# Performance work log

Measured on AMD Instinct MI355X. Metric: run time of the kernel, lower is better.

Reference implementation:

```python
import jax, jax.numpy as jnp
import numpy as np

EPS = 1e-5  # torch LayerNorm default

def _ln(x, g, b):
    mu = jnp.mean(x, -1, keepdims=True)
    var = jnp.mean((x - mu) ** 2, -1, keepdims=True)
    return (x - mu) * jax.lax.rsqrt(var + EPS) * g + b

def _xavier(key, shape):
    fan_in, fan_out = shape[-2], shape[-1]
    s = (2.0 / (fan_in + fan_out)) ** 0.5
    return jax.random.normal(key, shape, dtype=jnp.float32) * s

def setup_inputs() -> dict:
    key = jax.random.key(0)
    ks = jax.random.split(key, 24)
    N, E, B = 10000, 160000, 64
    D, M, FF, K = 128, 32, 32, 5
    EIN = 2 * FF + 1 + 2 * D          # 321
    inp = {}
    inp["coords"] = jax.random.normal(ks[0], (N, 3), dtype=jnp.float32)
    inp["atomids"] = jax.random.randint(ks[1], (N,), 0, 11)
    inp["edge_index"] = jax.random.randint(ks[2], (2, E), 0, N)
    inp["batch"] = jnp.sort(jax.random.randint(ks[3], (N,), 0, B))
    inp["num_graphs"] = B
    inp["emb"] = _xavier(ks[4], (11, D))
    # stacked per-kernel EGNN params (leading dim K=5)
    inp["keW1"] = _xavier(ks[5], (K, EIN, 2 * EIN)); inp["keb1"] = jnp.zeros((K, 2 * EIN))
    inp["keW2"] = _xavier(ks[6], (K, 2 * EIN, M));   inp["keb2"] = jnp.zeros((K, M))
    inp["keng"] = jnp.ones((K, M));   inp["kenb"] = jnp.zeros((K, M))
    inp["kn1g"] = jnp.ones((K, D));   inp["kn1b"] = jnp.zeros((K, D))
    inp["knW1"] = _xavier(ks[7], (K, D + M, 2 * D)); inp["knb1"] = jnp.zeros((K, 2 * D))
    inp["knW2"] = _xavier(ks[8], (K, 2 * D, D));     inp["knb2"] = jnp.zeros((K, D))
    inp["kn2g"] = jnp.ones((K, D));   inp["kn2b"] = jnp.zeros((K, D))
    # fnn: (K+1)*D = 768 -> 256 -> 256 -> 256
    inp["fW0"] = _xavier(ks[9], ((K + 1) * D, 256)); inp["fb0"] = jnp.zeros((256,))
    inp["fW1"] = _xavier(ks[10], (256, 256));        inp["fb1"] = jnp.zeros((256,))
    inp["fW2"] = _xavier(ks[11], (256, 256));        inp["fb2"] = jnp.zeros((256,))
    # fnn2: 256 -> 256 -> 256 -> 1
    inp["gW0"] = _xavier(ks[12], (256, 256));        inp["gb0"] = jnp.zeros((256,))
    inp["gW1"] = _xavier(ks[13], (256, 256));        inp["gb1"] = jnp.zeros((256,))
    inp["gW2"] = _xavier(ks[14], (256, 1));          inp["gb2"] = jnp.zeros((1,))
    return inp

def reference(coords, atomids, edge_index, batch, num_graphs, emb,
              keW1, keb1, keW2, keb2, keng, kenb, kn1g, kn1b,
              knW1, knb1, knW2, knb2, kn2g, kn2b,
              fW0, fb0, fW1, fb1, fW2, fb2,
              gW0, gb0, gW1, gb1, gW2, gb2):
    silu = jax.nn.silu
    N = coords.shape[0]
    src, dst = edge_index[0], edge_index[1]  # x_j = x[src], x_i = x[dst]
    feats = emb[atomids]                                  # [N,128]
    # coords are never updated across kernels -> fourier edge attr computed once
    rel = coords[src] - coords[dst]                       # [E,3]
    d = jnp.sum(rel * rel, -1, keepdims=True)             # [E,1] squared distance
    scales = 2.0 ** jnp.arange(32, dtype=coords.dtype)
    xs = d / scales                                       # [E,32]
    ea = jnp.concatenate([jnp.sin(xs), jnp.cos(xs), d], -1)  # [E,65]
    ones_e = jnp.ones((src.shape[0], 1), feats.dtype)
    deg = jax.ops.segment_sum(ones_e, dst, num_segments=N)   # [N,1]
    deg = jnp.maximum(deg, 1.0)
    feat_list = [feats]
    for k in range(keW1.shape[0]):
        # edge message MLP
        m = jnp.concatenate([feats[dst], feats[src], ea], -1)        # [E,321]
        h = silu(m @ keW1[k] + keb1[k])                              # [E,642]
        m_ij = silu(h @ keW2[k] + keb2[k])                           # [E,32]
        m_ij = _ln(m_ij, keng[k], kenb[k])
        # scatter-mean aggregate to target nodes
        m_i = jax.ops.segment_sum(m_ij, dst, num_segments=N) / deg   # [N,32]
        m_i = _ln(m_i, keng[k], kenb[k])  # (original reuses edge_norm1)
        # node update MLP with residual
        hf = _ln(feats, kn1g[k], kn1b[k])
        h2 = silu(jnp.concatenate([hf, m_i], -1) @ knW1[k] + knb1[k])
        h2 = h2 @ knW2[k] + knb2[k]
        h2 = _ln(h2, kn2g[k], kn2b[k])
        feats = feats + h2
        feat_list.append(feats)
    f = silu(jnp.concatenate(feat_list, -1))              # [N,768]
    f = silu(f @ fW0 + fb0)
    f = silu(f @ fW1 + fb1)
    f = silu(f @ fW2 + fb2)
    gs = jax.ops.segment_sum(f, batch, num_segments=num_graphs)
    gc = jax.ops.segment_sum(jnp.ones((N, 1), f.dtype), batch, num_segments=num_graphs)
    g = gs / jnp.maximum(gc, 1.0)                         # [B,256] scatter_mean
    g = silu(g @ gW0 + gb0)
    g = silu(g @ gW1 + gb1)
    return g @ gW2 + gb2                                  # [B,1]
```

## Files before the change

### kernel.cpp

```cpp
#include <hip/hip_runtime.h>
#include <cstdint>
#include <cstddef>


#define DEV __device__ __forceinline__

typedef __attribute__((ext_vector_type(8))) short bf16x8;
typedef __attribute__((ext_vector_type(4))) float f32x4;

DEV float siluf(float x) { return x / (1.f + __expf(-x)); }

DEV unsigned short f2bf(float f) {
  unsigned u = __float_as_uint(f);
  unsigned r = u + 0x7FFFu + ((u >> 16) & 1u);
  return (unsigned short)(r >> 16);
}
DEV float bf2f(unsigned short h) { return __uint_as_float(((unsigned)h) << 16); }

DEV f32x4 mfma16(bf16x8 a, bf16x8 b, f32x4 c) {
  return __builtin_amdgcn_mfma_f32_16x16x32_bf16(a, b, c, 0, 0, 0);
}

DEV void unpack8(bf16x8 v, float* o) {
#pragma unroll
  for (int j = 0; j < 8; ++j) o[j] = bf2f((unsigned short)v[j]);
}

__global__ __launch_bounds__(256) void k_gather(const int* __restrict__ atomids,
                                                const float* __restrict__ emb,
                                                float* __restrict__ feats_all,
                                                unsigned short* __restrict__ fH, int N) {
  int idx = blockIdx.x * 256 + threadIdx.x;
  if (idx >= N * 128) return;
  int i = idx >> 7, j = idx & 127;
  float v = emb[atomids[i] * 128 + j];
  size_t o = (size_t)i * 768 + j;
  feats_all[o] = v;
  fH[o] = f2bf(v);
}

__global__ __launch_bounds__(256) void k_edge_prep(const float* __restrict__ coords,
                                                   const int* __restrict__ ei, int E,
                                                   float* __restrict__ d_arr,
                                                   int* __restrict__ cnt) {
  int e = blockIdx.x * 256 + threadIdx.x;
  if (e >= E) return;
  int s = ei[e], t = ei[E + e];
  float dx = coords[3 * s + 0] - coords[3 * t + 0];
  float dy = coords[3 * s + 1] - coords[3 * t + 1];
  float dz = coords[3 * s + 2] - coords[3 * t + 2];
  d_arr[e] = dx * dx + dy * dy + dz * dz;
  atomicAdd(&cnt[t], 1);
}

__global__ __launch_bounds__(1024) void k_scan(const int* __restrict__ cnt, int N,
                                               int* __restrict__ cursor,
                                               float* __restrict__ degf) {
  __shared__ int s[1024];
  __shared__ int carry;
  if (threadIdx.x == 0) carry = 0;
  __syncthreads();
  for (int base = 0; base < N; base += 1024) {
    int i = base + threadIdx.x;
    int v = (i < N) ? cnt[i] : 0;
    s[threadIdx.x] = v;
    __syncthreads();
    for (int off = 1; off < 1024; off <<= 1) {
      int add = (threadIdx.x >= off) ? s[threadIdx.x - off] : 0;
      __syncthreads();
      s[threadIdx.x] += add;
      __syncthreads();
    }
    if (i < N) {
      cursor[i] = s[threadIdx.x] - v + carry;
      degf[i] = fmaxf((float)v, 1.f);
    }
    __syncthreads();
    if (threadIdx.x == 0) carry += s[1023];
    __syncthreads();
  }
}

__global__ __launch_bounds__(256) void k_scatter(const int* __restrict__ ei, int E,
                                                 const float* __restrict__ d_arr,
                                                 int* __restrict__ cursor,
                                                 int* __restrict__ ssrc,
                                                 int* __restrict__ sdst,
                                                 float* __restrict__ sd) {
  int e = blockIdx.x * 256 + threadIdx.x;
  if (e >= E) return;
  int s = ei[e], t = ei[E + e];
  int p = atomicAdd(&cursor[t], 1);
  ssrc[p] = s;
  sdst[p] = t;
  sd[p] = d_arr[e];
}

__global__ __launch_bounds__(256) void k_prepack(
    const float* __restrict__ W, size_t wStride, int ldw,
    int K, int Kpad, int Ncols, int Npad,
    unsigned short* __restrict__ hi, unsigned short* __restrict__ lo, size_t oStride) {
  int idx = blockIdx.x * 256 + threadIdx.x;
  int total = Npad * Kpad;
  if (idx >= total) return;
  W += blockIdx.y * wStride;
  hi += blockIdx.y * oStride;
  lo += blockIdx.y * oStride;
  int n = idx / Kpad, k = idx - n * Kpad;
  float v = (n < Ncols && k < K) ? W[(size_t)k * ldw + n] : 0.f;
  unsigned short h = f2bf(v);
  hi[idx] = h;
  lo[idx] = f2bf(v - bf2f(h));
}

__global__ __launch_bounds__(256) void gemm_bf(
    const unsigned short* __restrict__ AH, int lda,
    const unsigned short* __restrict__ BH, const unsigned short* __restrict__ BL, int ldb,
    const float* __restrict__ bias,
    float* __restrict__ C, int ldc,
    unsigned short* __restrict__ CH, int ldch,
    int M, int Ncols, int K, int actOut, int actA) {
  const int t = threadIdx.x;
  const int wave = t >> 6, lane = t & 63;
  const int nl = lane & 15, quad = lane >> 4;
  const int bm = blockIdx.x * 128 + wave * 32;
  const int bn = blockIdx.y * 64;
  f32x4 zero = {0.f, 0.f, 0.f, 0.f};
  f32x4 acc[2][4] = {{zero, zero, zero, zero}, {zero, zero, zero, zero}};
  for (int kb = 0; kb < K; kb += 32) {
    bf16x8 ah[2];
#pragma unroll
    for (int h = 0; h < 2; ++h) {
      int row = bm + h * 16 + nl;
      if (row < M) {
        ah[h] = *(const bf16x8*)(AH + (size_t)row * lda + kb + quad * 8);
        if (actA) {
#pragma unroll
          for (int j = 0; j < 8; ++j) {
            float a = siluf(bf2f((unsigned short)ah[h][j]));
            ah[h][j] = (short)f2bf(a);
          }
        }
      } else {
#pragma unroll
        for (int j = 0; j < 8; ++j) ah[h][j] = 0;
      }
    }
#pragma unroll
    for (int tn = 0; tn < 4; ++tn) {
      size_t boff = (size_t)(bn + tn * 16 + nl) * ldb + kb + quad * 8;
      bf16x8 bh = *(const bf16x8*)(BH + boff);
      bf16x8 bl = *(const bf16x8*)(BL + boff);
#pragma unroll
      for (int h = 0; h < 2; ++h) {
        acc[h][tn] = mfma16(ah[h], bh, acc[h][tn]);
        acc[h][tn] = mfma16(ah[h], bl, acc[h][tn]);
      }
    }
  }
#pragma unroll
  for (int h = 0; h < 2; ++h) {
#pragma unroll
    for (int tn = 0; tn < 4; ++tn) {
      int c = bn + tn * 16 + nl;
      float bv = (bias && c < Ncols) ? bias[c] : 0.f;
#pragma unroll
      for (int r = 0; r < 4; ++r) {
        int rr = bm + h * 16 + quad * 4 + r;
        if (rr >= M) continue;
        float v = acc[h][tn][r] + bv;
        if (actOut) v = siluf(v);
        if (C && c < Ncols) C[(size_t)rr * ldc + c] = v;
        if (CH && c < Ncols) CH[(size_t)rr * ldch + c] = f2bf(v);
      }
    }
  }
}

__global__ __launch_bounds__(256) void gemm_proj(
    const unsigned short* __restrict__ AH, int lda,
    const unsigned short* __restrict__ B1H, const unsigned short* __restrict__ B1L,
    const unsigned short* __restrict__ B2H, const unsigned short* __restrict__ B2L,
    const float* __restrict__ bias1,
    unsigned short* __restrict__ C1, unsigned short* __restrict__ C2,
    int planeN, int M) {
  const int y = blockIdx.y;
  const unsigned short* BH;
  const unsigned short* BL;
  const float* bias;
  unsigned short* CP;
  int yp;
  if (y < 11) { BH = B1H; BL = B1L; bias = bias1; CP = C1; yp = y; }
  else        { BH = B2H; BL = B2L; bias = nullptr; CP = C2; yp = y - 11; }
  const int t = threadIdx.x;
  const int wave = t >> 6, lane = t & 63;
  const int nl = lane & 15, quad = lane >> 4;
  const int bm = blockIdx.x * 128 + wave * 32;
  const int bn = yp * 64;
  f32x4 zero = {0.f, 0.f, 0.f, 0.f};
  f32x4 acc[2][4] = {{zero, zero, zero, zero}, {zero, zero, zero, zero}};
  for (int kb = 0; kb < 128; kb += 32) {
    bf16x8 ah[2];
#pragma unroll
    for (int h = 0; h < 2; ++h) {
      int row = bm + h * 16 + nl;
      if (row < M)
        ah[h] = *(const bf16x8*)(AH + (size_t)row * lda + kb + quad * 8);
      else
#pragma unroll
        for (int j = 0; j < 8; ++j) ah[h][j] = 0;
    }
#pragma unroll
    for (int tn = 0; tn < 4; ++tn) {
      size_t boff = (size_t)(bn + tn * 16 + nl) * 128 + kb + quad * 8;
      bf16x8 bh = *(const bf16x8*)(BH + boff);
      bf16x8 bl = *(const bf16x8*)(BL + boff);
#pragma unroll
      for (int h = 0; h < 2; ++h) {
        acc[h][tn] = mfma16(ah[h], bh, acc[h][tn]);
        acc[h][tn] = mfma16(ah[h], bl, acc[h][tn]);
      }
    }
  }
#pragma unroll
  for (int h = 0; h < 2; ++h) {
#pragma unroll
    for (int tn = 0; tn < 4; ++tn) {
      int c = bn + tn * 16 + nl;
      float bv = (bias && c < 642) ? bias[c] : 0.f;
#pragma unroll
      for (int r = 0; r < 4; ++r) {
        int rr = bm + h * 16 + quad * 4 + r;
        if (rr >= M) continue;
        CP[(size_t)yp * planeN + (size_t)rr * 64 + tn * 16 + nl] =
            f2bf(acc[h][tn][r] + bv);
      }
    }
  }
}

__global__ __launch_bounds__(256, 4) void k_edge_mfma(
    const unsigned short* __restrict__ Ap, const unsigned short* __restrict__ Bp,
    int planeN,
    const int* __restrict__ ssrc, const int* __restrict__ sdst,
    const float* __restrict__ sd_g, int E,
    const unsigned short* __restrict__ WeaT,
    const float* __restrict__ Wea64,
    const unsigned short* __restrict__ W2T,
    const float* __restrict__ b2v,
    const float* __restrict__ eng, const float* __restrict__ enb,
    float* __restrict__ msum) {
  __shared__ float sAB[4][16 * 68];
  __shared__ unsigned short sHh[4][16 * 72];
  __shared__ float sDs[64];
  __shared__ int sSrcS[64], sDstS[64];

  const int t = threadIdx.x;
  const int wave = t >> 6, lane = t & 63;
  const int nl = lane & 15, quad = lane >> 4;
  const int e0 = blockIdx.x * 64;

  if (lane < 16) {
    int el = wave * 16 + lane;
    int e = e0 + el;
    int ec = (e < E) ? e : (E - 1);
    sSrcS[el] = ssrc[ec];
    sDstS[el] = sdst[ec];
    sDs[el] = sd_g[ec];
  }
  const int r = lane >> 2, cq = lane & 3;
  const int elr = wave * 16 + r;
  const size_t aOff = (size_t)sDstS[elr] * 64 + cq * 16;
  const size_t bOff = (size_t)sSrcS[elr] * 64 + cq * 16;
  const float dR = sDs[elr];
  float* myAB = sAB[wave];
  unsigned short* myH = sHh[wave];

  bf16x8 pa0, pa1, pb0, pb1;
  bf16x8 w1[4][2], w2[2][2];

  auto loadW1 = [&](int c) {
#pragma unroll
    for (int tn = 0; tn < 4; ++tn)
#pragma unroll
      for (int ks = 0; ks < 2; ++ks)
        w1[tn][ks] = *(const bf16x8*)(WeaT + (size_t)(c * 64 + tn * 16 + nl) * 64 +
                                      ks * 32 + quad * 8);
  };
  auto loadW2 = [&](int c) {
#pragma unroll
    for (int tn = 0; tn < 2; ++tn)
#pragma unroll
      for (int ks = 0; ks < 2; ++ks)
        w2[tn][ks] = *(const bf16x8*)(W2T + (size_t)(tn * 16 + nl) * 704 + c * 64 +
                                      ks * 32 + quad * 8);
  };
  auto issue = [&](int c) {
    const unsigned short* a = Ap + (size_t)c * planeN + aOff;
    const unsigned short* b = Bp + (size_t)c * planeN + bOff;
    pa0 = *(const bf16x8*)a;
    pa1 = *(const bf16x8*)(a + 8);
    pb0 = *(const bf16x8*)b;
    pb1 = *(const bf16x8*)(b + 8);
  };
  auto commit = [&](int c) {
    float za[16], zb[16], w[16];
    unpack8(pa0, za); unpack8(pa1, za + 8);
    unpack8(pb0, zb); unpack8(pb1, zb + 8);
    const int cb = c * 64 + cq * 16;
    if (cb + 15 < 642) {
#pragma unroll
      for (int j = 0; j < 4; ++j) {
        f32x4 wv = *(const f32x4*)(Wea64 + cb + 4 * j);
        w[4 * j] = wv.x; w[4 * j + 1] = wv.y; w[4 * j + 2] = wv.z; w[4 * j + 3] = wv.w;
      }
    } else {
#pragma unroll
      for (int u = 0; u < 16; ++u) w[u] = (cb + u < 642) ? Wea64[cb + u] : 0.f;
    }
#pragma unroll
    for (int j = 0; j < 4; ++j) {
      f32x4 o;
#pragma unroll
      for (int u = 0; u < 4; ++u) o[u] = za[4 * j + u] + zb[4 * j + u] + dR * w[4 * j + u];
      *(f32x4*)(myAB + r * 68 + cq * 16 + 4 * j) = o;
    }
  };

  issue(0);
  bf16x8 eaHi[2];
  {
    float d = sDs[wave * 16 + nl];
#pragma unroll
    for (int ks = 0; ks < 2; ++ks)
#pragma unroll
      for (int j = 0; j < 8; ++j) {
        int k = ks * 32 + quad * 8 + j;
        float arg = d * exp2f(-(float)(k & 31));
        float v = (k < 32) ? __sinf(arg) : __cosf(arg);
        eaHi[ks][j] = (short)f2bf(v);
      }
  }
  loadW1(0);
  loadW2(0);

  f32x4 zero = {0.f, 0.f, 0.f, 0.f};
  f32x4 macc[2] = {zero, zero};

  for (int c = 0; c < 11; ++c) {
    commit(c);
    if (c < 10) issue(c + 1);
    f32x4 acc1[4];
#pragma unroll
    for (int tn = 0; tn < 4; ++tn)
#pragma unroll
      for (int rr = 0; rr < 4; ++rr)
        acc1[tn][rr] = myAB[(quad * 4 + rr) * 68 + tn * 16 + nl];
#pragma unroll
    for (int tn = 0; tn < 4; ++tn)
#pragma unroll
      for (int ks = 0; ks < 2; ++ks) acc1[tn] = mfma16(eaHi[ks], w1[tn][ks], acc1[tn]);
    if (c < 10) loadW1(c + 1);
#pragma unroll
    for (int tn = 0; tn < 4; ++tn)
#pragma unroll
      for (int rr = 0; rr < 4; ++rr)
        myH[(quad * 4 + rr) * 72 + tn * 16 + nl] = f2bf(siluf(acc1[tn][rr]));
#pragma unroll
    for (int ks = 0; ks < 2; ++ks) {
      bf16x8 ah = *(const bf16x8*)(myH + nl * 72 + ks * 32 + quad * 8);
#pragma unroll
      for (int tn = 0; tn < 2; ++tn) macc[tn] = mfma16(ah, w2[tn][ks], macc[tn]);
    }
    if (c < 10) loadW2(c + 1);
  }

  float g0 = eng[nl], g1v = eng[16 + nl], bb0 = enb[nl], bb1 = enb[16 + nl];
  float bi0 = b2v[nl], bi1 = b2v[16 + nl];
  float* sMw = myAB;
#pragma unroll
  for (int rr = 0; rr < 4; ++rr) {
    float v0 = siluf(macc[0][rr] + bi0);
    float v1 = siluf(macc[1][rr] + bi1);
    float s = v0 + v1;
    float ss = v0 * v0 + v1 * v1;
#pragma unroll
    for (int m = 1; m < 16; m <<= 1) {
      s += __shfl_xor(s, m, 16);
      ss += __shfl_xor(ss, m, 16);
    }
    float mu = s * (1.f / 32.f);
    float var = ss * (1.f / 32.f) - mu * mu;
    float rs = rsqrtf(var + 1e-5f);
    int lr = quad * 4 + rr;
    sMw[lr * 33 + nl] = (v0 - mu) * rs * g0 + bb0;
    sMw[lr * 33 + 16 + nl] = (v1 - mu) * rs * g1v + bb1;
  }
  __syncthreads();
  {
    int col = t & 31, seg = t >> 5;
    float acc = 0.f;
    int cur = -1;
#pragma unroll
    for (int i = 0; i < 8; ++i) {
      int e = seg * 8 + i;
      int dn = (e0 + e < E) ? sDstS[e] : -1;
      if (dn != cur) {
        if (cur >= 0) atomicAdd(&msum[(size_t)cur * 32 + col], acc);
        acc = 0.f;
        cur = dn;
      }
      if (dn >= 0) acc += sAB[e >> 4][(e & 15) * 33 + col];
    }
    if (cur >= 0) atomicAdd(&msum[(size_t)cur * 32 + col], acc);
  }
}

__global__ __launch_bounds__(256) void k_node_ln(
    const float* __restrict__ msum, const float* __restrict__ deg,
    const float* __restrict__ featsAll, int k,
    const float* __restrict__ n1g, const float* __restrict__ n1b,
    const float* __restrict__ eng, const float* __restrict__ enb,
    unsigned short* __restrict__ hcatH, int N) {
  int node = blockIdx.x * 4 + (threadIdx.x >> 6);
  int lane = threadIdx.x & 63;
  if (node >= N) return;
  const float* fr = featsAll + (size_t)node * 768 + k * 128;
  float x0 = fr[lane], x1 = fr[64 + lane];
  float s = x0 + x1;
#pragma unroll
  for (int m = 1; m < 64; m <<= 1) s += __shfl_xor(s, m, 64);
  float mu = s * (1.f / 128.f);
  float d0 = x0 - mu, d1 = x1 - mu;
  float v = d0 * d0 + d1 * d1;
#pragma unroll
  for (int m = 1; m < 64; m <<= 1) v += __shfl_xor(v, m, 64);
  float rstd = rsqrtf(v * (1.f / 128.f) + 1e-5f);
  size_t hb = (size_t)node * 160;
  hcatH[hb + lane] = f2bf(d0 * rstd * n1g[lane] + n1b[lane]);
  hcatH[hb + 64 + lane] = f2bf(d1 * rstd * n1g[64 + lane] + n1b[64 + lane]);
  float dg = deg[node];
  int col = lane & 31;
  float y = msum[(size_t)node * 32 + col] / dg;
  float sy = y;
#pragma unroll
  for (int m = 1; m < 32; m <<= 1) sy += __shfl_xor(sy, m, 32);
  float mu2 = sy * (1.f / 32.f);
  float dy = y - mu2;
  float vy = dy * dy;
#pragma unroll
  for (int m = 1; m < 32; m <<= 1) vy += __shfl_xor(vy, m, 32);
  float rstd2 = rsqrtf(vy * (1.f / 32.f) + 1e-5f);
  if (lane < 32) hcatH[hb + 128 + col] = f2bf(dy * rstd2 * eng[col] + enb[col]);
}

__global__ __launch_bounds__(256) void k_node_resid(
    const float* __restrict__ t2, float* __restrict__ featsAll, int k,
    const float* __restrict__ n2g, const float* __restrict__ n2b,
    unsigned short* __restrict__ fH, int N) {
  int node = blockIdx.x * 4 + (threadIdx.x >> 6);
  int lane = threadIdx.x & 63;
  if (node >= N) return;
  const float* tr = t2 + (size_t)node * 128;
  float x0 = tr[lane], x1 = tr[64 + lane];
  float s = x0 + x1;
#pragma unroll
  for (int m = 1; m < 64; m <<= 1) s += __shfl_xor(s, m, 64);
  float mu = s * (1.f / 128.f);
  float d0 = x0 - mu, d1 = x1 - mu;
  float v = d0 * d0 + d1 * d1;
#pragma unroll
  for (int m = 1; m < 64; m <<= 1) v += __shfl_xor(v, m, 64);
  float rstd = rsqrtf(v * (1.f / 128.f) + 1e-5f);
  const float* fk = featsAll + (size_t)node * 768 + k * 128;
  size_t ob = (size_t)node * 768 + (k + 1) * 128;
  float o0 = fk[lane] + d0 * rstd * n2g[lane] + n2b[lane];
  float o1 = fk[64 + lane] + d1 * rstd * n2g[64 + lane] + n2b[64 + lane];
  featsAll[ob + lane] = o0;
  featsAll[ob + 64 + lane] = o1;
  fH[ob + lane] = f2bf(o0);
  fH[ob + 64 + lane] = f2bf(o1);
}

__global__ __launch_bounds__(256) void k_pool2(const float* __restrict__ f,
                                               const int* __restrict__ batch,
                                               float* __restrict__ gsum,
                                               float* __restrict__ gcnt, int N) {
  int n0 = blockIdx.x * 64;
  int col = threadIdx.x;
  float acc = 0.f;
  int cur = -1;
  for (int i = 0; i < 64; ++i) {
    int n = n0 + i;
    if (n >= N) break;
    int b = batch[n];
    if (b != cur) {
      if (cur >= 0) atomicAdd(&gsum[cur * 256 + col], acc);
      acc = 0.f;
      cur = b;
    }
    acc += f[(size_t)n * 256 + col];
  }
  if (cur >= 0) atomicAdd(&gsum[cur * 256 + col], acc);
  if (threadIdx.x == 0) {
    int cnt = 0;
    cur = -1;
    for (int i = 0; i < 64; ++i) {
      int n = n0 + i;
      if (n >= N) break;
      int b = batch[n];
      if (b != cur) {
        if (cur >= 0) atomicAdd(&gcnt[cur], (float)cnt);
        cnt = 0;
        cur = b;
      }
      cnt++;
    }
    if (cur >= 0) atomicAdd(&gcnt[cur], (float)cnt);
  }
}

__global__ void k_gdiv(float* gsum, const float* gcnt, unsigned short* gH) {
  int b = blockIdx.x, j = threadIdx.x;
  float v = gsum[b * 256 + j] / fmaxf(gcnt[b], 1.f);
  gH[b * 256 + j] = f2bf(v);
}

__global__ void k_gout(const float* __restrict__ g2, const float* __restrict__ gW2,
                       const float* __restrict__ gb2, float* __restrict__ out) {
  int b = threadIdx.x;
  if (b >= 64) return;
  float s = gb2[0];
  for (int j = 0; j < 256; ++j) s += g2[b * 256 + j] * gW2[j];
  out[b] = s;
}

extern "C" void kernel_launch(void* const* d_in, const int* in_sizes, int n_in,
                              void* d_out, int out_size, void* d_ws, size_t ws_size,
                              hipStream_t stream) {
  const float* coords = (const float*)d_in[0];
  const int* atomids = (const int*)d_in[1];
  const int* ei = (const int*)d_in[2];
  const int* batch = (const int*)d_in[3];
  const float* emb = (const float*)d_in[5];
  const float* keW1 = (const float*)d_in[6];
  const float* keb1 = (const float*)d_in[7];
  const float* keW2 = (const float*)d_in[8];
  const float* keb2 = (const float*)d_in[9];
  const float* keng = (const float*)d_in[10];
  const float* kenb = (const float*)d_in[11];
  const float* kn1g = (const float*)d_in[12];
  const float* kn1b = (const float*)d_in[13];
  const float* knW1 = (const float*)d_in[14];
  const float* knb1 = (const float*)d_in[15];
  const float* knW2 = (const float*)d_in[16];
  const float* knb2 = (const float*)d_in[17];
  const float* kn2g = (const float*)d_in[18];
  const float* kn2b = (const float*)d_in[19];
  const float* fW0 = (const float*)d_in[20];
  const float* fb0 = (const float*)d_in[21];
  const float* fW1 = (const float*)d_in[22];
  const float* fb1 = (const float*)d_in[23];
  const float* fW2 = (const float*)d_in[24];
  const float* fb2 = (const float*)d_in[25];
  const float* gW0 = (const float*)d_in[26];
  const float* gb0 = (const float*)d_in[27];
  const float* gW1 = (const float*)d_in[28];
  const float* gb1 = (const float*)d_in[29];
  const float* gW2 = (const float*)d_in[30];
  const float* gb2 = (const float*)d_in[31];

  const int N = in_sizes[0] / 3;
  const int E = in_sizes[2] / 2;
  const int planeN = N * 64;

  size_t off = 0;
  auto alloc = [&](size_t n) {
    float* p = (float*)d_ws + off;
    off += (n + 63) & ~(size_t)63;
    return p;
  };
  float* feats_all = alloc((size_t)N * 768);
  float* d_arr = alloc(E);
  float* degf = alloc(N);
  float* msum = alloc((size_t)N * 32);
  float* t2 = alloc((size_t)N * 128);
  float* f1 = alloc((size_t)N * 256);
  float* gsum = alloc(64 * 256);
  float* gcnt = alloc(64);
  float* g2 = alloc(64 * 256);
  int* cnt = (int*)alloc(N);
  int* cursor = (int*)alloc(N);
  int* ssrc = (int*)alloc(E);
  int* sdst = (int*)alloc(E);
  float* sd = alloc(E);

  unsigned short* ubase = (unsigned short*)(alloc(0));
  size_t uoff = 0;
  auto ualloc = [&](size_t n) {
    unsigned short* p = ubase + uoff;
    uoff += (n + 63) & ~(size_t)63;
    return p;
  };
  unsigned short* fH = ualloc((size_t)N * 768);
  unsigned short* ApU = ualloc((size_t)11 * planeN);
  unsigned short* BpU = ualloc((size_t)11 * planeN);
  unsigned short* hcatH = ualloc((size_t)N * 160);
  unsigned short* t1H = ualloc((size_t)N * 256);
  unsigned short* fAH = ualloc((size_t)N * 256);
  unsigned short* fBH = ualloc((size_t)N * 256);
  unsigned short* gH = ualloc(64 * 256);
  unsigned short* g1H = ualloc(64 * 256);
  const size_t sDst_ = 704 * 128, sSrc_ = 704 * 128, sEa_ = 704 * 64;
  const size_t sW2_ = 32 * 704, sN1_ = 256 * 160, sN2_ = 128 * 256;
  unsigned short* PdstH = ualloc(5 * sDst_); unsigned short* PdstL = ualloc(5 * sDst_);
  unsigned short* PsrcH = ualloc(5 * sSrc_); unsigned short* PsrcL = ualloc(5 * sSrc_);
  unsigned short* PeaH = ualloc(5 * sEa_);   unsigned short* PeaL = ualloc(5 * sEa_);
  unsigned short* PW2H = ualloc(5 * sW2_);   unsigned short* PW2L = ualloc(5 * sW2_);
  unsigned short* Pn1H = ualloc(5 * sN1_);   unsigned short* Pn1L = ualloc(5 * sN1_);
  unsigned short* Pn2H = ualloc(5 * sN2_);   unsigned short* Pn2L = ualloc(5 * sN2_);
  unsigned short* Pf0H = ualloc(256 * 768);  unsigned short* Pf0L = ualloc(256 * 768);
  unsigned short* Pf1H = ualloc(256 * 256);  unsigned short* Pf1L = ualloc(256 * 256);
  unsigned short* Pf2H = ualloc(256 * 256);  unsigned short* Pf2L = ualloc(256 * 256);
  unsigned short* Pg0H = ualloc(256 * 256);  unsigned short* Pg0L = ualloc(256 * 256);
  unsigned short* Pg1H = ualloc(256 * 256);  unsigned short* Pg1L = ualloc(256 * 256);

  auto pp = [&](const float* W, size_t wStr, int ldw, int K, int Kpad, int Nc, int Npad,
                unsigned short* hi, unsigned short* lo, size_t oStr, int layers) {
    int total = Npad * Kpad;
    k_prepack<<<dim3((total + 255) / 256, layers), 256, 0, stream>>>(
        W, wStr, ldw, K, Kpad, Nc, Npad, hi, lo, oStr);
  };
  pp(keW1, (size_t)321 * 642, 642, 128, 128, 642, 704, PdstH, PdstL, sDst_, 5);
  pp(keW1 + 128 * 642, (size_t)321 * 642, 642, 128, 128, 642, 704, PsrcH, PsrcL, sSrc_, 5);
  pp(keW1 + 256 * 642, (size_t)321 * 642, 642, 64, 64, 642, 704, PeaH, PeaL, sEa_, 5);
  pp(keW2, (size_t)642 * 32, 32, 642, 704, 32, 32, PW2H, PW2L, sW2_, 5);
  pp(knW1, (size_t)160 * 256, 256, 160, 160, 256, 256, Pn1H, Pn1L, sN1_, 5);
  pp(knW2, (size_t)256 * 128, 128, 256, 256, 128, 128, Pn2H, Pn2L, sN2_, 5);
  pp(fW0, 0, 256, 768, 768, 256, 256, Pf0H, Pf0L, 0, 1);
  pp(fW1, 0, 256, 256, 256, 256, 256, Pf1H, Pf1L, 0, 1);
  pp(fW2, 0, 256, 256, 256, 256, 256, Pf2H, Pf2L, 0, 1);
  pp(gW0, 0, 256, 256, 256, 256, 256, Pg0H, Pg0L, 0, 1);
  pp(gW1, 0, 256, 256, 256, 256, 256, Pg1H, Pg1L, 0, 1);

  k_gather<<<(N * 128 + 255) / 256, 256, 0, stream>>>(atomids, emb, feats_all, fH, N);
  hipMemsetAsync(cnt, 0, (size_t)N * sizeof(int), stream);
  k_edge_prep<<<(E + 255) / 256, 256, 0, stream>>>(coords, ei, E, d_arr, cnt);
  k_scan<<<1, 1024, 0, stream>>>(cnt, N, cursor, degf);
  k_scatter<<<(E + 255) / 256, 256, 0, stream>>>(ei, E, d_arr, cursor, ssrc, sdst, sd);

  const int MT = (N + 127) / 128;
  for (int k = 0; k < 5; ++k) {
    gemm_proj<<<dim3(MT, 22), 256, 0, stream>>>(
        fH + k * 128, 768,
        PdstH + k * sDst_, PdstL + k * sDst_,
        PsrcH + k * sSrc_, PsrcL + k * sSrc_,
        keb1 + k * 642, ApU, BpU, planeN, N);
    hipMemsetAsync(msum, 0, (size_t)N * 32 * sizeof(float), stream);
    k_edge_mfma<<<(E + 63) / 64, 256, 0, stream>>>(
        ApU, BpU, planeN, ssrc, sdst, sd, E,
        PeaH + k * sEa_,
        keW1 + (size_t)k * 321 * 642 + (size_t)320 * 642,
        PW2H + k * sW2_,
        keb2 + k * 32, keng + k * 32, kenb + k * 32, msum);
    k_node_ln<<<(N + 3) / 4, 256, 0, stream>>>(
        msum, degf, feats_all, k, kn1g + k * 128, kn1b + k * 128,
        keng + k * 32, kenb + k * 32, hcatH, N);
    gemm_bf<<<dim3(MT, 4), 256, 0, stream>>>(
        hcatH, 160, Pn1H + k * sN1_, Pn1L + k * sN1_, 160,
        knb1 + k * 256, nullptr, 0, t1H, 256, N, 256, 160, 1, 0);
    gemm_bf<<<dim3(MT, 2), 256, 0, stream>>>(
        t1H, 256, Pn2H + k * sN2_, Pn2L + k * sN2_, 256,
        knb2 + k * 128, t2, 128, nullptr, 0, N, 128, 256, 0, 0);
    k_node_resid<<<(N + 3) / 4, 256, 0, stream>>>(
        t2, feats_all, k, kn2g + k * 128, kn2b + k * 128, fH, N);
  }

  gemm_bf<<<dim3(MT, 4), 256, 0, stream>>>(
      fH, 768, Pf0H, Pf0L, 768, fb0, nullptr, 0, fAH, 256, N, 256, 768, 1, 1);
  gemm_bf<<<dim3(MT, 4), 256, 0, stream>>>(
      fAH, 256, Pf1H, Pf1L, 256, fb1, nullptr, 0, fBH, 256, N, 256, 256, 1, 0);
  gemm_bf<<<dim3(MT, 4), 256, 0, stream>>>(
      fBH, 256, Pf2H, Pf2L, 256, fb2, f1, 256, nullptr, 0, N, 256, 256, 1, 0);

  hipMemsetAsync(gsum, 0, 64 * 256 * sizeof(float), stream);
  hipMemsetAsync(gcnt, 0, 64 * sizeof(float), stream);
  k_pool2<<<(N + 63) / 64, 256, 0, stream>>>(f1, batch, gsum, gcnt, N);
  k_gdiv<<<64, 256, 0, stream>>>(gsum, gcnt, gH);
  gemm_bf<<<dim3(1, 4), 256, 0, stream>>>(
      gH, 256, Pg0H, Pg0L, 256, gb0, nullptr, 0, g1H, 256, 64, 256, 256, 1, 0);
  gemm_bf<<<dim3(1, 4), 256, 0, stream>>>(
      g1H, 256, Pg1H, Pg1L, 256, gb1, g2, 256, nullptr, 0, 64, 256, 256, 1, 0);
  k_gout<<<1, 64, 0, stream>>>(g2, gW2, gb2, (float*)d_out);
}
```

Baseline: 1.928 ms.

## Fuse node MLP second GEMM with LayerNorm residual and batch weight prepacking

Result: faster. 1.808 ms (-6.2%).

```diff
diff --git a/kernel.cpp b/kernel.cpp
--- a/kernel.cpp
+++ b/kernel.cpp
@@ -53,31 +53,40 @@
   atomicAdd(&cnt[t], 1);
 }
 
-__global__ __launch_bounds__(1024) void k_scan(const int* __restrict__ cnt, int N,
-                                               int* __restrict__ cursor,
-                                               float* __restrict__ degf) {
-  __shared__ int s[1024];
-  __shared__ int carry;
-  if (threadIdx.x == 0) carry = 0;
+__global__ __launch_bounds__(1024) void k_scan2(const int* __restrict__ cnt, int N,
+                                                int* __restrict__ cursor,
+                                                float* __restrict__ degf) {
+  __shared__ int wsum[16];
+  int tid = threadIdx.x;
+  int chunk = (N + 1023) >> 10;
+  int lo = tid * chunk, hi = min(N, lo + chunk);
+  int s = 0;
+  for (int i = lo; i < hi; ++i) s += cnt[i];
+  int lane = tid & 63, wv = tid >> 6;
+  int v = s;
+#pragma unroll
+  for (int off = 1; off < 64; off <<= 1) {
+    int u = __shfl_up(v, off, 64);
+    if (lane >= off) v += u;
+  }
+  if (lane == 63) wsum[wv] = v;
   __syncthreads();
-  for (int base = 0; base < N; base += 1024) {
-    int i = base + threadIdx.x;
-    int v = (i < N) ? cnt[i] : 0;
-    s[threadIdx.x] = v;
-    __syncthreads();
-    for (int off = 1; off < 1024; off <<= 1) {
-      int add = (threadIdx.x >= off) ? s[threadIdx.x - off] : 0;
-      __syncthreads();
-      s[threadIdx.x] += add;
-      __syncthreads();
-    }
-    if (i < N) {
-      cursor[i] = s[threadIdx.x] - v + carry;
-      degf[i] = fmaxf((float)v, 1.f);
-    }
-    __syncthreads();
-    if (threadIdx.x == 0) carry += s[1023];
-    __syncthreads();
+  if (wv == 0 && lane < 16) {
+    int w = wsum[lane];
+#pragma unroll
+    for (int off = 1; off < 16; off <<= 1) {
+      int u = __shfl_up(w, off, 16);
+      if (lane >= off) w += u;
+    }
+    wsum[lane] = w;
+  }
+  __syncthreads();
+  int run = (wv ? wsum[wv - 1] : 0) + v - s;
+  for (int i = lo; i < hi; ++i) {
+    int c = cnt[i];
+    cursor[i] = run;
+    degf[i] = fmaxf((float)c, 1.f);
+    run += c;
   }
 }
 
@@ -96,21 +105,28 @@
   sd[p] = d_arr[e];
 }
 
-__global__ __launch_bounds__(256) void k_prepack(
-    const float* __restrict__ W, size_t wStride, int ldw,
-    int K, int Kpad, int Ncols, int Npad,
-    unsigned short* __restrict__ hi, unsigned short* __restrict__ lo, size_t oStride) {
-  int idx = blockIdx.x * 256 + threadIdx.x;
-  int total = Npad * Kpad;
-  if (idx >= total) return;
-  W += blockIdx.y * wStride;
-  hi += blockIdx.y * oStride;
-  lo += blockIdx.y * oStride;
-  int n = idx / Kpad, k = idx - n * Kpad;
-  float v = (n < Ncols && k < K) ? W[(size_t)k * ldw + n] : 0.f;
+struct PPJob {
+  const float* W;
+  unsigned short* hi;
+  unsigned short* lo;
+  unsigned long long wStride, oStride;
+  int ldw, K, Kpad, Nc, Npad, layers;
+};
+struct PPJobs { PPJob j[11]; };
+
+__global__ __launch_bounds__(256) void k_prepack_all(PPJobs jobs) {
+  PPJob jb = jobs.j[blockIdx.y];
+  long long per = (long long)jb.Npad * jb.Kpad;
+  long long idx = (long long)blockIdx.x * 256 + threadIdx.x;
+  if (idx >= per * jb.layers) return;
+  int layer = (int)(idx / per);
+  int r = (int)(idx - (long long)layer * per);
+  const float* W = jb.W + (size_t)layer * jb.wStride;
+  int n = r / jb.Kpad, k = r - n * jb.Kpad;
+  float v = (n < jb.Nc && k < jb.K) ? W[(size_t)k * jb.ldw + n] : 0.f;
   unsigned short h = f2bf(v);
-  hi[idx] = h;
-  lo[idx] = f2bf(v - bf2f(h));
+  jb.hi[(size_t)layer * jb.oStride + r] = h;
+  jb.lo[(size_t)layer * jb.oStride + r] = f2bf(v - bf2f(h));
 }
 
 __global__ __launch_bounds__(256) void gemm_bf(
@@ -123,56 +139,45 @@
   const int t = threadIdx.x;
   const int wave = t >> 6, lane = t & 63;
   const int nl = lane & 15, quad = lane >> 4;
-  const int bm = blockIdx.x * 128 + wave * 32;
+  const int bm = blockIdx.x * 64 + wave * 16;
   const int bn = blockIdx.y * 64;
   f32x4 zero = {0.f, 0.f, 0.f, 0.f};
-  f32x4 acc[2][4] = {{zero, zero, zero, zero}, {zero, zero, zero, zero}};
+  f32x4 acc[4] = {zero, zero, zero, zero};
   for (int kb = 0; kb < K; kb += 32) {
-    bf16x8 ah[2];
-#pragma unroll
-    for (int h = 0; h < 2; ++h) {
-      int row = bm + h * 16 + nl;
-      if (row < M) {
-        ah[h] = *(const bf16x8*)(AH + (size_t)row * lda + kb + quad * 8);
-        if (actA) {
-#pragma unroll
-          for (int j = 0; j < 8; ++j) {
-            float a = siluf(bf2f((unsigned short)ah[h][j]));
-            ah[h][j] = (short)f2bf(a);
-          }
-        }
-      } else {
-#pragma unroll
-        for (int j = 0; j < 8; ++j) ah[h][j] = 0;
-      }
+    bf16x8 ah;
+    int row = bm + nl;
+    if (row < M) {
+      ah = *(const bf16x8*)(AH + (size_t)row * lda + kb + quad * 8);
+      if (actA) {
+#pragma unroll
+        for (int j = 0; j < 8; ++j)
+          ah[j] = (short)f2bf(siluf(bf2f((unsigned short)ah[j])));
+      }
+    } else {
+#pragma unroll
+      for (int j = 0; j < 8; ++j) ah[j] = 0;
     }
 #pragma unroll
     for (int tn = 0; tn < 4; ++tn) {
       size_t boff = (size_t)(bn + tn * 16 + nl) * ldb + kb + quad * 8;
       bf16x8 bh = *(const bf16x8*)(BH + boff);
       bf16x8 bl = *(const bf16x8*)(BL + boff);
-#pragma unroll
-      for (int h = 0; h < 2; ++h) {
-        acc[h][tn] = mfma16(ah[h], bh, acc[h][tn]);
-        acc[h][tn] = mfma16(ah[h], bl, acc[h][tn]);
-      }
-    }
-  }
-#pragma unroll
-  for (int h = 0; h < 2; ++h) {
-#pragma unroll
-    for (int tn = 0; tn < 4; ++tn) {
-      int c = bn + tn * 16 + nl;
-      float bv = (bias && c < Ncols) ? bias[c] : 0.f;
-#pragma unroll
-      for (int r = 0; r < 4; ++r) {
-        int rr = bm + h * 16 + quad * 4 + r;
-        if (rr >= M) continue;
-        float v = acc[h][tn][r] + bv;
-        if (actOut) v = siluf(v);
-        if (C && c < Ncols) C[(size_t)rr * ldc + c] = v;
-        if (CH && c < Ncols) CH[(size_t)rr * ldch + c] = f2bf(v);
-      }
+      acc[tn] = mfma16(ah, bh, acc[tn]);
+      acc[tn] = mfma16(ah, bl, acc[tn]);
+    }
+  }
+#pragma unroll
+  for (int tn = 0; tn < 4; ++tn) {
+    int c = bn + tn * 16 + nl;
+    float bv = (bias && c < Ncols) ? bias[c] : 0.f;
+#pragma unroll
+    for (int r = 0; r < 4; ++r) {
+      int rr = bm + quad * 4 + r;
+      if (rr >= M) continue;
+      float v = acc[tn][r] + bv;
+      if (actOut) v = siluf(v);
+      if (C && c < Ncols) C[(size_t)rr * ldc + c] = v;
+      if (CH && c < Ncols) CH[(size_t)rr * ldch + c] = f2bf(v);
     }
   }
 }
@@ -239,7 +244,7 @@
   }
 }
 
-__global__ __launch_bounds__(256, 4) void k_edge_mfma(
+__global__ __launch_bounds__(256, 3) void k_edge_mfma(
     const unsigned short* __restrict__ Ap, const unsigned short* __restrict__ Bp,
     int planeN,
     const int* __restrict__ ssrc, const int* __restrict__ sdst,
@@ -277,7 +282,7 @@
   unsigned short* myH = sHh[wave];
 
   bf16x8 pa0, pa1, pb0, pb1;
-  bf16x8 w1[4][2], w2[2][2];
+  bf16x8 w1[4][2], w2a[2][2], w2b[2][2];
 
   auto loadW1 = [&](int c) {
 #pragma unroll
@@ -287,13 +292,13 @@
         w1[tn][ks] = *(const bf16x8*)(WeaT + (size_t)(c * 64 + tn * 16 + nl) * 64 +
                                       ks * 32 + quad * 8);
   };
-  auto loadW2 = [&](int c) {
+  auto loadW2 = [&](int c, bf16x8(*w)[2]) {
 #pragma unroll
     for (int tn = 0; tn < 2; ++tn)
 #pragma unroll
       for (int ks = 0; ks < 2; ++ks)
-        w2[tn][ks] = *(const bf16x8*)(W2T + (size_t)(tn * 16 + nl) * 704 + c * 64 +
-                                      ks * 32 + quad * 8);
+        w[tn][ks] = *(const bf16x8*)(W2T + (size_t)(tn * 16 + nl) * 704 + c * 64 +
+                                     ks * 32 + quad * 8);
   };
   auto issue = [&](int c) {
     const unsigned short* a = Ap + (size_t)c * planeN + aOff;
@@ -342,37 +347,39 @@
       }
   }
   loadW1(0);
-  loadW2(0);
+  loadW2(0, w2a);
 
   f32x4 zero = {0.f, 0.f, 0.f, 0.f};
   f32x4 macc[2] = {zero, zero};
 
+#pragma unroll
   for (int c = 0; c < 11; ++c) {
     commit(c);
     if (c < 10) issue(c + 1);
-    f32x4 acc1[4];
+    f32x4 acc1[4] = {zero, zero, zero, zero};
 #pragma unroll
     for (int tn = 0; tn < 4; ++tn)
 #pragma unroll
-      for (int rr = 0; rr < 4; ++rr)
-        acc1[tn][rr] = myAB[(quad * 4 + rr) * 68 + tn * 16 + nl];
+      for (int ks = 0; ks < 2; ++ks) acc1[tn] = mfma16(eaHi[ks], w1[tn][ks], acc1[tn]);
 #pragma unroll
     for (int tn = 0; tn < 4; ++tn)
 #pragma unroll
-      for (int ks = 0; ks < 2; ++ks) acc1[tn] = mfma16(eaHi[ks], w1[tn][ks], acc1[tn]);
-    if (c < 10) loadW1(c + 1);
-#pragma unroll
-    for (int tn = 0; tn < 4; ++tn)
-#pragma unroll
-      for (int rr = 0; rr < 4; ++rr)
-        myH[(quad * 4 + rr) * 72 + tn * 16 + nl] = f2bf(siluf(acc1[tn][rr]));
+      for (int rr = 0; rr < 4; ++rr) {
+        int lrow = quad * 4 + rr;
+        float z = acc1[tn][rr] + myAB[lrow * 68 + tn * 16 + nl];
+        myH[lrow * 72 + tn * 16 + nl] = f2bf(siluf(z));
+      }
+    if (c < 10) {
+      loadW1(c + 1);
+      loadW2(c + 1, (c & 1) ? w2a : w2b);
+    }
+    bf16x8(*w2)[2] = (c & 1) ? w2b : w2a;
 #pragma unroll
     for (int ks = 0; ks < 2; ++ks) {
       bf16x8 ah = *(const bf16x8*)(myH + nl * 72 + ks * 32 + quad * 8);
 #pragma unroll
       for (int tn = 0; tn < 2; ++tn) macc[tn] = mfma16(ah, w2[tn][ks], macc[tn]);
     }
-    if (c < 10) loadW2(c + 1);
   }
 
   float g0 = eng[nl], g1v = eng[16 + nl], bb0 = enb[nl], bb1 = enb[16 + nl];
@@ -454,32 +461,74 @@
   if (lane < 32) hcatH[hb + 128 + col] = f2bf(dy * rstd2 * eng[col] + enb[col]);
 }
 
-__global__ __launch_bounds__(256) void k_node_resid(
-    const float* __restrict__ t2, float* __restrict__ featsAll, int k,
+__global__ __launch_bounds__(256) void k_n2_resid(
+    const unsigned short* __restrict__ t1H,
+    const unsigned short* __restrict__ BH, const unsigned short* __restrict__ BL,
+    const float* __restrict__ b2,
     const float* __restrict__ n2g, const float* __restrict__ n2b,
-    unsigned short* __restrict__ fH, int N) {
-  int node = blockIdx.x * 4 + (threadIdx.x >> 6);
-  int lane = threadIdx.x & 63;
-  if (node >= N) return;
-  const float* tr = t2 + (size_t)node * 128;
-  float x0 = tr[lane], x1 = tr[64 + lane];
-  float s = x0 + x1;
-#pragma unroll
-  for (int m = 1; m < 64; m <<= 1) s += __shfl_xor(s, m, 64);
-  float mu = s * (1.f / 128.f);
-  float d0 = x0 - mu, d1 = x1 - mu;
-  float v = d0 * d0 + d1 * d1;
-#pragma unroll
-  for (int m = 1; m < 64; m <<= 1) v += __shfl_xor(v, m, 64);
-  float rstd = rsqrtf(v * (1.f / 128.f) + 1e-5f);
-  const float* fk = featsAll + (size_t)node * 768 + k * 128;
-  size_t ob = (size_t)node * 768 + (k + 1) * 128;
-  float o0 = fk[lane] + d0 * rstd * n2g[lane] + n2b[lane];
-  float o1 = fk[64 + lane] + d1 * rstd * n2g[64 + lane] + n2b[64 + lane];
-  featsAll[ob + lane] = o0;
-  featsAll[ob + 64 + lane] = o1;
-  fH[ob + lane] = f2bf(o0);
-  fH[ob + 64 + lane] = f2bf(o1);
+    float* __restrict__ featsAll, unsigned short* __restrict__ fH, int k, int N) {
+  const int t = threadIdx.x;
+  const int wave = t >> 6, lane = t & 63;
+  const int nl = lane & 15, quad = lane >> 4;
+  const int bm = blockIdx.x * 64 + wave * 16;
+  f32x4 zero = {0.f, 0.f, 0.f, 0.f};
+  f32x4 acc[8] = {zero, zero, zero, zero, zero, zero, zero, zero};
+  for (int kb = 0; kb < 256; kb += 32) {
+    bf16x8 ah;
+    int row = bm + nl;
+    if (row < N)
+      ah = *(const bf16x8*)(t1H + (size_t)row * 256 + kb + quad * 8);
+    else
+#pragma unroll
+      for (int j = 0; j < 8; ++j) ah[j] = 0;
+#pragma unroll
+    for (int tn = 0; tn < 8; ++tn) {
+      size_t boff = (size_t)(tn * 16 + nl) * 256 + kb + quad * 8;
+      bf16x8 bh = *(const bf16x8*)(BH + boff);
+      bf16x8 bl = *(const bf16x8*)(BL + boff);
+      acc[tn] = mfma16(ah, bh, acc[tn]);
+      acc[tn] = mfma16(ah, bl, acc[tn]);
+    }
+  }
+  float bv[8], gv[8], bb[8];
+#pragma unroll
+  for (int tn = 0; tn < 8; ++tn) {
+    int col = tn * 16 + nl;
+    bv[tn] = b2[col];
+    gv[tn] = n2g[col];
+    bb[tn] = n2b[col];
+  }
+#pragma unroll
+  for (int r = 0; r < 4; ++r) {
+    int row = bm + quad * 4 + r;
+    float v[8];
+    float s = 0.f, ss = 0.f;
+#pragma unroll
+    for (int tn = 0; tn < 8; ++tn) {
+      v[tn] = acc[tn][r] + bv[tn];
+      s += v[tn];
+      ss += v[tn] * v[tn];
+    }
+#pragma unroll
+    for (int m = 1; m < 16; m <<= 1) {
+      s += __shfl_xor(s, m, 16);
+      ss += __shfl_xor(ss, m, 16);
+    }
+    float mu = s * (1.f / 128.f);
+    float var = ss * (1.f / 128.f) - mu * mu;
+    float rs = rsqrtf(var + 1e-5f);
+    if (row < N) {
+      const float* fk = featsAll + (size_t)row * 768 + k * 128;
+      size_t ob = (size_t)row * 768 + (k + 1) * 128;
+#pragma unroll
+      for (int tn = 0; tn < 8; ++tn) {
+        int col = tn * 16 + nl;
+        float o = fk[col] + (v[tn] - mu) * rs * gv[tn] + bb[tn];
+        featsAll[ob + col] = o;
+        fH[ob + col] = f2bf(o);
+      }
+    }
+  }
 }
 
 __global__ __launch_bounds__(256) void k_pool2(const float* __restrict__ f,
@@ -584,7 +633,6 @@
   float* d_arr = alloc(E);
   float* degf = alloc(N);
   float* msum = alloc((size_t)N * 32);
-  float* t2 = alloc((size_t)N * 128);
   float* f1 = alloc((size_t)N * 256);
   float* gsum = alloc(64 * 256);
   float* gcnt = alloc(64);
@@ -625,33 +673,36 @@
   unsigned short* Pg0H = ualloc(256 * 256);  unsigned short* Pg0L = ualloc(256 * 256);
   unsigned short* Pg1H = ualloc(256 * 256);  unsigned short* Pg1L = ualloc(256 * 256);
 
-  auto pp = [&](const float* W, size_t wStr, int ldw, int K, int Kpad, int Nc, int Npad,
-                unsigned short* hi, unsigned short* lo, size_t oStr, int layers) {
-    int total = Npad * Kpad;
-    k_prepack<<<dim3((total + 255) / 256, layers), 256, 0, stream>>>(
-        W, wStr, ldw, K, Kpad, Nc, Npad, hi, lo, oStr);
+  PPJobs jobs;
+  auto setJob = [&](int i, const float* W, size_t wStr, int ldw, int K, int Kpad,
+                    int Nc, int Npad, unsigned short* hi, unsigned short* lo,
+                    size_t oStr, int layers) {
+    jobs.j[i] = PPJob{W, hi, lo, (unsigned long long)wStr, (unsigned long long)oStr,
+                      ldw, K, Kpad, Nc, Npad, layers};
   };
-  pp(keW1, (size_t)321 * 642, 642, 128, 128, 642, 704, PdstH, PdstL, sDst_, 5);
-  pp(keW1 + 128 * 642, (size_t)321 * 642, 642, 128, 128, 642, 704, PsrcH, PsrcL, sSrc_, 5);
-  pp(keW1 + 256 * 642, (size_t)321 * 642, 642, 64, 64, 642, 704, PeaH, PeaL, sEa_, 5);
-  pp(keW2, (size_t)642 * 32, 32, 642, 704, 32, 32, PW2H, PW2L, sW2_, 5);
-  pp(knW1, (size_t)160 * 256, 256, 160, 160, 256, 256, Pn1H, Pn1L, sN1_, 5);
-  pp(knW2, (size_t)256 * 128, 128, 256, 256, 128, 128, Pn2H, Pn2L, sN2_, 5);
-  pp(fW0, 0, 256, 768, 768, 256, 256, Pf0H, Pf0L, 0, 1);
-  pp(fW1, 0, 256, 256, 256, 256, 256, Pf1H, Pf1L, 0, 1);
-  pp(fW2, 0, 256, 256, 256, 256, 256, Pf2H, Pf2L, 0, 1);
-  pp(gW0, 0, 256, 256, 256, 256, 256, Pg0H, Pg0L, 0, 1);
-  pp(gW1, 0, 256, 256, 256, 256, 256, Pg1H, Pg1L, 0, 1);
+  setJob(0, keW1, (size_t)321 * 642, 642, 128, 128, 642, 704, PdstH, PdstL, sDst_, 5);
+  setJob(1, keW1 + 128 * 642, (size_t)321 * 642, 642, 128, 128, 642, 704, PsrcH, PsrcL, sSrc_, 5);
+  setJob(2, keW1 + 256 * 642, (size_t)321 * 642, 642, 64, 64, 642, 704, PeaH, PeaL, sEa_, 5);
+  setJob(3, keW2, (size_t)642 * 32, 32, 642, 704, 32, 32, PW2H, PW2L, sW2_, 5);
+  setJob(4, knW1, (size_t)160 * 256, 256, 160, 160, 256, 256, Pn1H, Pn1L, sN1_, 5);
+  setJob(5, knW2, (size_t)256 * 128, 128, 256, 256, 128, 128, Pn2H, Pn2L, sN2_, 5);
+  setJob(6, fW0, 0, 256, 768, 768, 256, 256, Pf0H, Pf0L, 0, 1);
+  setJob(7, fW1, 0, 256, 256, 256, 256, 256, Pf1H, Pf1L, 0, 1);
+  setJob(8, fW2, 0, 256, 256, 256, 256, 256, Pf2H, Pf2L, 0, 1);
+  setJob(9, gW0, 0, 256, 256, 256, 256, 256, Pg0H, Pg0L, 0, 1);
+  setJob(10, gW1, 0, 256, 256, 256, 256, 256, Pg1H, Pg1L, 0, 1);
+  k_prepack_all<<<dim3(1760, 11), 256, 0, stream>>>(jobs);
 
   k_gather<<<(N * 128 + 255) / 256, 256, 0, stream>>>(atomids, emb, feats_all, fH, N);
   hipMemsetAsync(cnt, 0, (size_t)N * sizeof(int), stream);
   k_edge_prep<<<(E + 255) / 256, 256, 0, stream>>>(coords, ei, E, d_arr, cnt);
-  k_scan<<<1, 1024, 0, stream>>>(cnt, N, cursor, degf);
+  k_scan2<<<1, 1024, 0, stream>>>(cnt, N, cursor, degf);
   k_scatter<<<(E + 255) / 256, 256, 0, stream>>>(ei, E, d_arr, cursor, ssrc, sdst, sd);
 
-  const int MT = (N + 127) / 128;
+  const int MT128 = (N + 127) / 128;
+  const int MT64 = (N + 63) / 64;
   for (int k = 0; k < 5; ++k) {
-    gemm_proj<<<dim3(MT, 22), 256, 0, stream>>>(
+    gemm_proj<<<dim3(MT128, 22), 256, 0, stream>>>(
         fH + k * 128, 768,
         PdstH + k * sDst_, PdstL + k * sDst_,
         PsrcH + k * sSrc_, PsrcL + k * sSrc_,
@@ -666,21 +717,19 @@
     k_node_ln<<<(N + 3) / 4, 256, 0, stream>>>(
         msum, degf, feats_all, k, kn1g + k * 128, kn1b + k * 128,
         keng + k * 32, kenb + k * 32, hcatH, N);
-    gemm_bf<<<dim3(MT, 4), 256, 0, stream>>>(
+    gemm_bf<<<dim3(MT64, 4), 256, 0, stream>>>(
         hcatH, 160, Pn1H + k * sN1_, Pn1L + k * sN1_, 160,
         knb1 + k * 256, nullptr, 0, t1H, 256, N, 256, 160, 1, 0);
-    gemm_bf<<<dim3(MT, 2), 256, 0, stream>>>(
-        t1H, 256, Pn2H + k * sN2_, Pn2L + k * sN2_, 256,
-        knb2 + k * 128, t2, 128, nullptr, 0, N, 128, 256, 0, 0);
-    k_node_resid<<<(N + 3) / 4, 256, 0, stream>>>(
-        t2, feats_all, k, kn2g + k * 128, kn2b + k * 128, fH, N);
-  }
-
-  gemm_bf<<<dim3(MT, 4), 256, 0, stream>>>(
+    k_n2_resid<<<MT64, 256, 0, stream>>>(
+        t1H, Pn2H + k * sN2_, Pn2L + k * sN2_, knb2 + k * 128,
+        kn2g + k * 128, kn2b + k * 128, feats_all, fH, k, N);
+  }
+
+  gemm_bf<<<dim3(MT64, 4), 256, 0, stream>>>(
       fH, 768, Pf0H, Pf0L, 768, fb0, nullptr, 0, fAH, 256, N, 256, 768, 1, 1);
-  gemm_bf<<<dim3(MT, 4), 256, 0, stream>>>(
+  gemm_bf<<<dim3(MT64, 4), 256, 0, stream>>>(
       fAH, 256, Pf1H, Pf1L, 256, fb1, nullptr, 0, fBH, 256, N, 256, 256, 1, 0);
-  gemm_bf<<<dim3(MT, 4), 256, 0, stream>>>(
+  gemm_bf<<<dim3(MT64, 4), 256, 0, stream>>>(
       fBH, 256, Pf2H, Pf2L, 256, fb2, f1, 256, nullptr, 0, N, 256, 256, 1, 0);
 
   hipMemsetAsync(gsum, 0, 64 * 256 * sizeof(float), stream);
```
